# Optimization experiments

Hardware: AMD Instinct MI355X
Metric: run time of the kernel (lower is better)

## Reference

```python
import jax, jax.numpy as jnp
import numpy as np

B, S, DIM, HEADS, HD, FF = 2, 2048, 1024, 16, 64, 4096
PREV, MAX_SEQ, THETA, POS_BIAS_MAX, EPS = 1024, 4096, 10000.0, 2.0, 1e-6


def _freqs_cos_sin():
    inv = 1.0 / THETA ** (np.arange(0, HD, 2)[: HD // 2].astype(np.float32) / HD)
    f = np.outer(np.arange(MAX_SEQ, dtype=np.float32), inv)
    return jnp.asarray(np.cos(f), jnp.float32), jnp.asarray(np.sin(f), jnp.float32)


def setup_inputs():
    key = jax.random.key(0)
    ks = jax.random.split(key, 16)
    lin = lambda k, o, i: 0.02 * jax.random.normal(k, (o, i), jnp.float32)
    cos, sin = _freqs_cos_sin()
    return {
        "x": jax.random.normal(ks[0], (B, S, DIM), jnp.float32),
        "cache_k": jax.random.normal(ks[1], (B, HEADS, PREV, HD), jnp.float32),
        "cache_v": jax.random.normal(ks[2], (B, HEADS, PREV, HD), jnp.float32),
        "cos": cos, "sin": sin,
        "attn_norm_w": jnp.ones((DIM,), jnp.float32),
        "ffn_norm_w": jnp.ones((DIM,), jnp.float32),
        "wq": lin(ks[3], DIM, DIM), "bq": jnp.zeros((DIM,), jnp.float32),
        "wk": lin(ks[4], DIM, DIM), "bk": jnp.zeros((DIM,), jnp.float32),
        "wv": lin(ks[5], DIM, DIM), "bv": jnp.zeros((DIM,), jnp.float32),
        "wo": lin(ks[6], DIM, DIM), "bo": jnp.zeros((DIM,), jnp.float32),
        "w_gate": lin(ks[7], FF, DIM), "b_gate": jnp.zeros((FF,), jnp.float32),
        "w_value": lin(ks[8], FF, DIM), "b_value": jnp.zeros((FF,), jnp.float32),
        "w_proj": lin(ks[9], DIM, FF), "b_proj": jnp.zeros((DIM,), jnp.float32),
        "cache_limit": 3072,
    }


def _rmsnorm(h, w):
    return h * jax.lax.rsqrt(jnp.mean(h * h, axis=-1, keepdims=True) + EPS) * w


def _rope(t, cos, sin):
    # t: [B,H,L,HD]; cos/sin: [L, HD//2]; rotate interleaved pairs (complex mult)
    t2 = t.reshape(t.shape[:-1] + (HD // 2, 2))
    x0, x1 = t2[..., 0], t2[..., 1]
    c = cos[None, None]
    s = sin[None, None]
    out = jnp.stack([x0 * c - x1 * s, x0 * s + x1 * c], axis=-1)
    return out.reshape(t.shape)


def _forward(x, cache_k, cache_v, cos, sin, attn_norm_w, ffn_norm_w, wq, bq, wk, bk, wv, bv, wo, bo, w_gate, b_gate, w_value, b_value, w_proj, b_proj, cache_limit):
    b, s, d = x.shape
    h = _rmsnorm(x, attn_norm_w)
    shape4 = lambda t: t.reshape(b, s, HEADS, HD).transpose(0, 2, 1, 3)  # [B,H,S,HD]
    q = shape4(h @ wq.T + bq)
    k_new = shape4(h @ wk.T + bk)
    v_new = shape4(h @ wv.T + bv)
    k_all = jnp.concatenate([cache_k, k_new], axis=2)
    v_all = jnp.concatenate([cache_v, v_new], axis=2)
    if cache_limit > 0:
        k_all = k_all[:, :, -cache_limit:, :]
        v_all = v_all[:, :, -cache_limit:, :]
    total = k_all.shape[2]
    prev = total - s
    # RoPE: q at absolute positions prev..prev+s-1, keys at 0..total-1 (mod cache len)
    pos_q = (jnp.arange(s) + prev) % MAX_SEQ
    pos_k = jnp.arange(total) % MAX_SEQ
    q = _rope(q, cos[pos_q], sin[pos_q])
    k = _rope(k_all, cos[pos_k], sin[pos_k])
    # linear positional bias + causal mask over the new-token block only
    slope = POS_BIAS_MAX / max(total - 1, 1)
    j = jnp.arange(total, dtype=jnp.float32)[None, :]
    i_abs = (prev + jnp.arange(s, dtype=jnp.float32))[:, None]
    bias = slope * (j - i_abs)  # [s, total]
    causal = (jnp.arange(total)[None, :] - prev) > jnp.arange(s)[:, None]
    mask = jnp.where(causal, -jnp.inf, bias)
    scores = jnp.einsum('bhsd,bhtd->bhst', q, k) / jnp.sqrt(jnp.float32(HD)) + mask
    attn = jax.nn.softmax(scores, axis=-1)
    ctx = jnp.einsum('bhst,bhtd->bhsd', attn, v_all)
    ctx = ctx.transpose(0, 2, 1, 3).reshape(b, s, d)
    x = x + ctx @ wo.T + bo
    h2 = _rmsnorm(x, ffn_norm_w)
    gated = jax.nn.silu(h2 @ w_gate.T + b_gate) * (h2 @ w_value.T + b_value)
    return x + gated @ w_proj.T + b_proj


def reference(x, cache_k, cache_v, cos, sin, attn_norm_w, ffn_norm_w, wq, bq, wk, bk, wv, bv, wo, bo, w_gate, b_gate, w_value, b_value, w_proj, b_proj, cache_limit):
    return _forward(x, cache_k, cache_v, cos, sin, attn_norm_w, ffn_norm_w, wq, bq, wk, bk, wv, bv, wo, bo, w_gate, b_gate, w_value, b_value, w_proj, b_proj, cache_limit)
```

## Files before the change

### kernel.cpp

```cpp
#include <hip/hip_runtime.h>
#include <stdint.h>

typedef unsigned short u16;
typedef unsigned int   u32;
typedef __bf16 bf16x8 __attribute__((ext_vector_type(8)));
typedef float  f32x4  __attribute__((ext_vector_type(4)));
typedef u32    u32x4  __attribute__((ext_vector_type(4)));
typedef u32    u32x2  __attribute__((ext_vector_type(2)));

#define B_SZ  2
#define S_LEN 2048
#define NH    16
#define HD    64
#define DIM   1024
#define FF    4096
#define T_LEN 3072
#define PREV  1024
#define MROWS (B_SZ * S_LEN)
#define LOG2E 1.44269504f

#define MFMA16 __builtin_amdgcn_mfma_f32_16x16x32_bf16

__device__ __forceinline__ u16 f2bf(float f) {
  u32 u = __builtin_bit_cast(u32, f);
  u32 r = u + 0x7FFFu + ((u >> 16) & 1u);
  return (u16)(r >> 16);
}
__device__ __forceinline__ float bf2f(u16 h) {
  u32 u = ((u32)h) << 16;
  return __builtin_bit_cast(float, u);
}
__device__ __forceinline__ u32 cvtpk(float lo, float hi) {
  u32 r;
  asm("v_cvt_pk_bf16_f32 %0, %1, %2" : "=v"(r) : "v"(lo), "v"(hi));
  return r;
}

__device__ __forceinline__ void gl_lds16(const void* g, void* l) {
  __builtin_amdgcn_global_load_lds(
      (const __attribute__((address_space(1))) u32*)g,
      (__attribute__((address_space(3))) u32*)l, 16, 0, 0);
}

__global__ __launch_bounds__(256) void cvt_kernel(const float* __restrict__ src,
                                                  u16* __restrict__ dst, int n4) {
  int i = blockIdx.x * 256 + threadIdx.x;
  const int stride = gridDim.x * 256;
  for (; i < n4; i += stride) {
    f32x4 v = *(const f32x4*)&src[(long)i * 4];
    u32x2 o;
    o[0] = (u32)f2bf(v[0]) | ((u32)f2bf(v[1]) << 16);
    o[1] = (u32)f2bf(v[2]) | ((u32)f2bf(v[3]) << 16);
    *(u32x2*)&dst[(long)i * 4] = o;
  }
}

__global__ __launch_bounds__(256) void cvt_ilv_kernel(const float* __restrict__ wg,
                                                      const float* __restrict__ wval,
                                                      u16* __restrict__ dst) {
  int i = blockIdx.x * 256 + threadIdx.x;
  const int stride = gridDim.x * 256;
  const int upr = DIM / 4;
  for (; i < FF * upr; i += stride) {
    int j = i / upr;
    int c = (i - j * upr) * 4;
    f32x4 g = *(const f32x4*)&wg[(long)j * DIM + c];
    f32x4 v = *(const f32x4*)&wval[(long)j * DIM + c];
    u32x2 og, ov;
    og[0] = (u32)f2bf(g[0]) | ((u32)f2bf(g[1]) << 16);
    og[1] = (u32)f2bf(g[2]) | ((u32)f2bf(g[3]) << 16);
    ov[0] = (u32)f2bf(v[0]) | ((u32)f2bf(v[1]) << 16);
    ov[1] = (u32)f2bf(v[2]) | ((u32)f2bf(v[3]) << 16);
    *(u32x2*)&dst[((long)2 * j) * DIM + c] = og;
    *(u32x2*)&dst[((long)2 * j + 1) * DIM + c] = ov;
  }
}

__global__ __launch_bounds__(256) void bias_ilv_kernel(const float* __restrict__ bg,
                                                       const float* __restrict__ bval,
                                                       float* __restrict__ dst) {
  int i = blockIdx.x * 256 + threadIdx.x;
  if (i < FF) {
    dst[2 * i] = bg[i];
    dst[2 * i + 1] = bval[i];
  }
}

__global__ __launch_bounds__(256) void rmsnorm_kernel(const float* __restrict__ x,
                                                      const float* __restrict__ w,
                                                      u16* __restrict__ out) {
  const int row = blockIdx.x;
  const int tid = threadIdx.x;
  const long base = (long)row * DIM + tid * 4;
  f32x4 v = *(const f32x4*)&x[base];
  float ss = v[0] * v[0] + v[1] * v[1] + v[2] * v[2] + v[3] * v[3];
#pragma unroll
  for (int d = 1; d <= 32; d <<= 1) ss += __shfl_xor(ss, d, 64);
  __shared__ float red[4];
  if ((tid & 63) == 0) red[tid >> 6] = ss;
  __syncthreads();
  float tot = red[0] + red[1] + red[2] + red[3];
  const float sc = rsqrtf(tot * (1.f / (float)DIM) + 1e-6f);
  f32x4 wv4 = *(const f32x4*)&w[tid * 4];
  u32x2 o;
  o[0] = (u32)f2bf(v[0] * sc * wv4[0]) | ((u32)f2bf(v[1] * sc * wv4[1]) << 16);
  o[1] = (u32)f2bf(v[2] * sc * wv4[2]) | ((u32)f2bf(v[3] * sc * wv4[3]) << 16);
  *(u32x2*)&out[base] = o;
}

template <int EPI>
__global__ __launch_bounds__(256) void gemm_bt(const u16* __restrict__ A,
                                               const u16* __restrict__ Bw,
                                               const float* __restrict__ bias,
                                               const float* __restrict__ resid,
                                               u16* __restrict__ out_bf,
                                               float* __restrict__ out_f,
                                               int N, int K) {
  __shared__ __align__(16) u16 As[2][128 * 32];
  __shared__ __align__(16) u16 Bs[2][128 * 32];
  const int tid = threadIdx.x;
  const int lane = tid & 63;
  const int wv = tid >> 6;
  const int wr = wv >> 1, wc = wv & 1;
  const long m0 = (long)blockIdx.y * 128;
  const long n0 = (long)blockIdx.x * 128;

  const int arow = tid >> 2;
  const int acol = (tid & 3) << 3;
  const u16* ag = A + (m0 + arow) * K + acol;
  const u16* bg = Bw + (n0 + arow) * K + acol;
  const long hK = (long)64 * K;

  f32x4 acc[4][4] = {};
  const int l15 = lane & 15;
  const int lhi = lane >> 4;
  const int aoff0 = (wr * 64 + l15) * 32 + lhi * 8;
  const int boff0 = (wc * 64 + l15) * 32 + lhi * 8;
  const int nk = K >> 5;

  gl_lds16(ag, &As[0][tid * 8]);
  gl_lds16(ag + hK, &As[0][2048 + tid * 8]);
  gl_lds16(bg, &Bs[0][tid * 8]);
  gl_lds16(bg + hK, &Bs[0][2048 + tid * 8]);
  __syncthreads();

  for (int t = 0; t < nk; ++t) {
    const int cur = t & 1, nxt = cur ^ 1;
    if (t + 1 < nk) {
      const int k1 = (t + 1) << 5;
      gl_lds16(ag + k1, &As[nxt][tid * 8]);
      gl_lds16(ag + k1 + hK, &As[nxt][2048 + tid * 8]);
      gl_lds16(bg + k1, &Bs[nxt][tid * 8]);
      gl_lds16(bg + k1 + hK, &Bs[nxt][2048 + tid * 8]);
    }
    bf16x8 af[4], bfr[4];
#pragma unroll
    for (int i = 0; i < 4; ++i) af[i] = *(const bf16x8*)&As[cur][aoff0 + i * 16 * 32];
#pragma unroll
    for (int j = 0; j < 4; ++j) bfr[j] = *(const bf16x8*)&Bs[cur][boff0 + j * 16 * 32];
    __builtin_amdgcn_s_setprio(1);
#pragma unroll
    for (int i = 0; i < 4; ++i)
#pragma unroll
      for (int j = 0; j < 4; ++j)
        acc[i][j] = MFMA16(af[i], bfr[j], acc[i][j], 0, 0, 0);
    __builtin_amdgcn_s_setprio(0);
    __syncthreads();
  }

#pragma unroll
  for (int i = 0; i < 4; ++i) {
    const long row0 = m0 + wr * 64 + i * 16 + lhi * 4;
#pragma unroll
    for (int j = 0; j < 4; ++j) {
      const long col = n0 + wc * 64 + j * 16 + l15;
      const float bb = bias[col];
#pragma unroll
      for (int r = 0; r < 4; ++r) {
        float v = acc[i][j][r] + bb;
        if (EPI == 2) {
          float other = __shfl_xor(v, 1, 64);
          if (!(l15 & 1)) {
            float s = v / (1.f + __expf(-v)) * other;
            out_bf[(row0 + r) * (N >> 1) + (col >> 1)] = f2bf(s);
          }
        } else {
          const long idx = (row0 + r) * N + col;
          if (EPI == 0) out_bf[idx] = f2bf(v);
          else          out_f[idx] = resid[idx] + v;
        }
      }
    }
  }
}

__global__ __launch_bounds__(256) void rope_q_kernel(const u16* __restrict__ qkv,
                                                     const float* __restrict__ cosT,
                                                     const float* __restrict__ sinT,
                                                     u16* __restrict__ Q) {
  int idx = blockIdx.x * 256 + threadIdx.x;
  int u = idx & 7;
  int s = (idx >> 3) & (S_LEN - 1);
  int bh = idx >> 14;
  int b = bh >> 4, h = bh & 15;
  int pos = PREV + s;
  const float SC = 0.125f * LOG2E;
  const u16* src = qkv + ((long)(b * S_LEN + s)) * (3 * DIM) + h * HD + u * 8;
  u32x4 d = *(const u32x4*)src;
  f32x4 cv = *(const f32x4*)&cosT[(long)pos * 32 + u * 4];
  f32x4 sv = *(const f32x4*)&sinT[(long)pos * 32 + u * 4];
  u32x4 o;
#pragma unroll
  for (int p = 0; p < 4; ++p) {
    float x0 = bf2f((u16)(d[p] & 0xffff));
    float x1 = bf2f((u16)(d[p] >> 16));
    float y0 = (x0 * cv[p] - x1 * sv[p]) * SC;
    float y1 = (x0 * sv[p] + x1 * cv[p]) * SC;
    o[p] = (u32)f2bf(y0) | ((u32)f2bf(y1) << 16);
  }
  *(u32x4*)&Q[((long)bh * S_LEN + s) * HD + u * 8] = o;
}

__global__ __launch_bounds__(256) void rope_k_kernel(const u16* __restrict__ qkv,
                                                     const float* __restrict__ cache_k,
                                                     const float* __restrict__ cosT,
                                                     const float* __restrict__ sinT,
                                                     u16* __restrict__ Kall) {
  int idx = blockIdx.x * 256 + threadIdx.x;
  int u = idx & 7;
  int t2 = idx >> 3;
  int j = t2 % T_LEN;
  int bh = t2 / T_LEN;
  int b = bh >> 4, h = bh & 15;
  float e[8];
  if (j < PREV) {
    const float* src = cache_k + ((long)bh * PREV + j) * HD + u * 8;
    f32x4 a = *(const f32x4*)src;
    f32x4 c = *(const f32x4*)(src + 4);
    e[0] = a[0]; e[1] = a[1]; e[2] = a[2]; e[3] = a[3];
    e[4] = c[0]; e[5] = c[1]; e[6] = c[2]; e[7] = c[3];
  } else {
    const u16* src = qkv + ((long)(b * S_LEN + (j - PREV))) * (3 * DIM) + DIM + h * HD + u * 8;
    u32x4 d = *(const u32x4*)src;
#pragma unroll
    for (int p = 0; p < 4; ++p) {
      e[2 * p] = bf2f((u16)(d[p] & 0xffff));
      e[2 * p + 1] = bf2f((u16)(d[p] >> 16));
    }
  }
  f32x4 cv = *(const f32x4*)&cosT[(long)j * 32 + u * 4];
  f32x4 sv = *(const f32x4*)&sinT[(long)j * 32 + u * 4];
  u32x4 o;
#pragma unroll
  for (int p = 0; p < 4; ++p) {
    float y0 = e[2 * p] * cv[p] - e[2 * p + 1] * sv[p];
    float y1 = e[2 * p] * sv[p] + e[2 * p + 1] * cv[p];
    o[p] = (u32)f2bf(y0) | ((u32)f2bf(y1) << 16);
  }
  *(u32x4*)&Kall[((long)bh * T_LEN + j) * HD + (u ^ (j & 7)) * 8] = o;
}

__global__ __launch_bounds__(256) void build_vt_kernel(const u16* __restrict__ qkv,
                                                       const float* __restrict__ cache_v,
                                                       u16* __restrict__ Vtg) {
  int idx = blockIdx.x * 256 + threadIdx.x;
  int hd = idx & 63;
  int t2 = idx >> 6;
  int kb = t2 % 384;
  int bh = t2 / 384;
  int b = bh >> 4, h = bh & 15;
  int key0 = kb * 8;
  u16 vals[8];
  if (key0 < PREV) {
#pragma unroll
    for (int i = 0; i < 8; ++i)
      vals[i] = f2bf(cache_v[((long)bh * PREV + key0 + i) * HD + hd]);
  } else {
#pragma unroll
    for (int i = 0; i < 8; ++i)
      vals[i] = qkv[((long)(b * S_LEN + key0 + i - PREV)) * (3 * DIM) + 2 * DIM + h * HD + hd];
  }
  u32x4 o;
#pragma unroll
  for (int p = 0; p < 4; ++p)
    o[p] = (u32)vals[2 * p] | ((u32)vals[2 * p + 1] << 16);
  const int span = kb >> 3;
  const int u = (kb & 7) ^ (hd & 7);
  *(u32x4*)&Vtg[((long)bh * HD + hd) * T_LEN + span * 64 + u * 8] = o;
}

__global__ __launch_bounds__(256, 4) void attn_kernel(const u16* __restrict__ Q,
                                                      const u16* __restrict__ Kg,
                                                      const u16* __restrict__ Vtg,
                                                      u16* __restrict__ ctx, float slope2) {
  __shared__ __align__(16) u16 Ks[2][64 * 64];
  __shared__ __align__(16) u16 Vs[2][64 * 64];
  __shared__ __align__(16) u16 Ps[4][16 * 64];

  const int tid = threadIdx.x;
  const int lane = tid & 63;
  const int wv = tid >> 6;
  const int l15 = lane & 15;
  const int lhi = lane >> 4;
  const int c7 = l15 & 7;
  const int bh = blockIdx.x;
  const int qt = blockIdx.y;
  const int b = bh >> 4, h = bh & 15;
  const int q0 = qt * 64;
  const int nt = (PREV + q0 + 64) >> 6;

  const long qrow = (long)bh * S_LEN + q0 + wv * 16 + l15;
  bf16x8 aq0 = *(const bf16x8*)&Q[qrow * HD + lhi * 8];
  bf16x8 aq1 = *(const bf16x8*)&Q[qrow * HD + 32 + lhi * 8];

  const long kgb = (long)bh * T_LEN * HD;
  const long vgb = (long)bh * HD * T_LEN;
  const int srow = tid >> 3;
  const int sunit = (tid & 7) * 8;

  gl_lds16(&Kg[kgb + (long)srow * HD + sunit], &Ks[0][tid * 8]);
  gl_lds16(&Kg[kgb + (long)(srow + 32) * HD + sunit], &Ks[0][2048 + tid * 8]);
  gl_lds16(&Vtg[vgb + (long)srow * T_LEN + sunit], &Vs[0][tid * 8]);
  gl_lds16(&Vtg[vgb + (long)(srow + 32) * T_LEN + sunit], &Vs[0][2048 + tid * 8]);
  __syncthreads();

  f32x4 o[4] = {};
  float mrun = -1e30f, lrun = 0.f;
  const int iabs = PREV + q0 + wv * 16 + l15;
  u16* Pw = &Ps[wv][0];

  for (int t = 0; t < nt; ++t) {
    const int cur = t & 1, nxt = cur ^ 1;
    const int kt0 = t << 6;
    if (t + 1 < nt) {
      const int kn = kt0 + 64;
      gl_lds16(&Kg[kgb + (long)(kn + srow) * HD + sunit], &Ks[nxt][tid * 8]);
      gl_lds16(&Kg[kgb + (long)(kn + srow + 32) * HD + sunit], &Ks[nxt][2048 + tid * 8]);
      gl_lds16(&Vtg[vgb + (long)srow * T_LEN + kn + sunit], &Vs[nxt][tid * 8]);
      gl_lds16(&Vtg[vgb + (long)(srow + 32) * T_LEN + kn + sunit], &Vs[nxt][2048 + tid * 8]);
    }

    f32x4 sf[4];
    __builtin_amdgcn_s_setprio(1);
#pragma unroll
    for (int jf = 0; jf < 4; ++jf) {
      const int krow = jf * 16 + l15;
      bf16x8 ak0 = *(const bf16x8*)&Ks[cur][krow * 64 + ((lhi ^ c7) * 8)];
      bf16x8 ak1 = *(const bf16x8*)&Ks[cur][krow * 64 + (((4 + lhi) ^ c7) * 8)];
      f32x4 s = {};
      s = MFMA16(ak0, aq0, s, 0, 0, 0);
      s = MFMA16(ak1, aq1, s, 0, 0, 0);
      sf[jf] = s;
    }
    __builtin_amdgcn_s_setprio(0);

    const bool masked = (t == nt - 1);
#pragma unroll
    for (int jf = 0; jf < 4; ++jf)
#pragma unroll
      for (int r = 0; r < 4; ++r) {
        const int jcol = kt0 + jf * 16 + 4 * lhi + r;
        float s_ = sf[jf][r] + slope2 * (float)(jcol - iabs);
        sf[jf][r] = (masked && jcol > iabs) ? -1e30f : s_;
      }

    float t0 = fmaxf(fmaxf(sf[0][0], sf[0][1]), fmaxf(sf[0][2], sf[0][3]));
    float t1 = fmaxf(fmaxf(sf[1][0], sf[1][1]), fmaxf(sf[1][2], sf[1][3]));
    float t2 = fmaxf(fmaxf(sf[2][0], sf[2][1]), fmaxf(sf[2][2], sf[2][3]));
    float t3 = fmaxf(fmaxf(sf[3][0], sf[3][1]), fmaxf(sf[3][2], sf[3][3]));
    float pmax = fmaxf(fmaxf(t0, t1), fmaxf(t2, t3));
    pmax = fmaxf(pmax, __shfl_xor(pmax, 16, 64));
    pmax = fmaxf(pmax, __shfl_xor(pmax, 32, 64));

    if (!__all(pmax - mrun <= 8.f)) {
      float mnew = fmaxf(mrun, pmax);
      float scl = exp2f(mrun - mnew);
      mrun = mnew;
      lrun *= scl;
#pragma unroll
      for (int r = 0; r < 4; ++r) {
        float sr = __shfl(scl, 4 * lhi + r, 64);
#pragma unroll
        for (int hf = 0; hf < 4; ++hf) o[hf][r] *= sr;
      }
    }

    float ps = 0.f;
#pragma unroll
    for (int jf = 0; jf < 4; ++jf) {
      f32x4 p;
#pragma unroll
      for (int r = 0; r < 4; ++r) {
        p[r] = exp2f(sf[jf][r] - mrun);
        ps += p[r];
      }
      u32x2 pw2;
      pw2[0] = cvtpk(p[0], p[1]);
      pw2[1] = cvtpk(p[2], p[3]);
      const int u = (2 * jf + (lhi >> 1)) ^ c7;
      *(u32x2*)&Pw[l15 * 64 + u * 8 + (lhi & 1) * 4] = pw2;
    }
    ps += __shfl_xor(ps, 16, 64);
    ps += __shfl_xor(ps, 32, 64);
    lrun += ps;

    bf16x8 pa0 = *(const bf16x8*)&Pw[l15 * 64 + ((lhi ^ c7) * 8)];
    bf16x8 pa1 = *(const bf16x8*)&Pw[l15 * 64 + (((4 + lhi) ^ c7) * 8)];
    __builtin_amdgcn_s_setprio(1);
#pragma unroll
    for (int hf = 0; hf < 4; ++hf) {
      const int vrow = hf * 16 + l15;
      bf16x8 bv0 = *(const bf16x8*)&Vs[cur][vrow * 64 + ((lhi ^ c7) * 8)];
      bf16x8 bv1 = *(const bf16x8*)&Vs[cur][vrow * 64 + (((4 + lhi) ^ c7) * 8)];
      o[hf] = MFMA16(pa0, bv0, o[hf], 0, 0, 0);
      o[hf] = MFMA16(pa1, bv1, o[hf], 0, 0, 0);
    }
    __builtin_amdgcn_s_setprio(0);
    __syncthreads();
  }

#pragma unroll
  for (int r = 0; r < 4; ++r) {
    const float inv = 1.f / __shfl(lrun, 4 * lhi + r, 64);
    const long srow_ = (long)b * S_LEN + q0 + wv * 16 + 4 * lhi + r;
#pragma unroll
    for (int hf = 0; hf < 4; ++hf)
      ctx[srow_ * DIM + h * HD + hf * 16 + l15] = f2bf(o[hf][r] * inv);
  }
}

extern "C" void kernel_launch(void* const* d_in, const int* in_sizes, int n_in,
                              void* d_out, int out_size, void* d_ws, size_t ws_size,
                              hipStream_t stream) {
  (void)in_sizes; (void)n_in; (void)out_size; (void)ws_size;
  const float* x       = (const float*)d_in[0];
  const float* cache_k = (const float*)d_in[1];
  const float* cache_v = (const float*)d_in[2];
  const float* cosT    = (const float*)d_in[3];
  const float* sinT    = (const float*)d_in[4];
  const float* attn_w  = (const float*)d_in[5];
  const float* ffn_w   = (const float*)d_in[6];
  const float* wq      = (const float*)d_in[7];
  const float* bq      = (const float*)d_in[8];
  const float* wk      = (const float*)d_in[9];
  const float* bk      = (const float*)d_in[10];
  const float* wv_     = (const float*)d_in[11];
  const float* bv      = (const float*)d_in[12];
  const float* wo      = (const float*)d_in[13];
  const float* bo      = (const float*)d_in[14];
  const float* wg      = (const float*)d_in[15];
  const float* bg      = (const float*)d_in[16];
  const float* wval    = (const float*)d_in[17];
  const float* bval    = (const float*)d_in[18];
  const float* wp      = (const float*)d_in[19];
  const float* bp      = (const float*)d_in[20];
  float* out = (float*)d_out;

  char* w = (char*)d_ws;
  size_t off = 0;
  auto alloc = [&](size_t bytes) -> char* {
    char* p = w + off;
    off += (bytes + 255) & ~(size_t)255;
    return p;
  };
  u16*   wqkv_bf  = (u16*)alloc((size_t)3 * DIM * DIM * 2);
  u16*   wo_bf    = (u16*)alloc((size_t)DIM * DIM * 2);
  u16*   wgv_bf   = (u16*)alloc((size_t)2 * FF * DIM * 2);
  u16*   wproj_bf = (u16*)alloc((size_t)DIM * FF * 2);
  float* bqkv     = (float*)alloc((size_t)3 * DIM * 4);
  float* bgv      = (float*)alloc((size_t)2 * FF * 4);
  float* x2       = (float*)alloc((size_t)MROWS * DIM * 4);
  char* AR = alloc((size_t)117440512);
  u16* qkv   = (u16*)(AR + 0);
  u16* Qb    = (u16*)(AR + 25165824);
  u16* Kb    = (u16*)(AR + 33554432);
  u16* Vtg   = (u16*)(AR + 46137344);
  u16* h1    = (u16*)(AR + 58720256);
  u16* ctx   = (u16*)(AR + 0);
  u16* h2    = (u16*)(AR + 8388608);
  u16* gated = (u16*)(AR + 16777216);

  cvt_kernel<<<512, 256, 0, stream>>>(wq, wqkv_bf, DIM * DIM / 4);
  cvt_kernel<<<512, 256, 0, stream>>>(wk, wqkv_bf + DIM * DIM, DIM * DIM / 4);
  cvt_kernel<<<512, 256, 0, stream>>>(wv_, wqkv_bf + 2 * DIM * DIM, DIM * DIM / 4);
  cvt_kernel<<<512, 256, 0, stream>>>(wo, wo_bf, DIM * DIM / 4);
  cvt_ilv_kernel<<<1024, 256, 0, stream>>>(wg, wval, wgv_bf);
  cvt_kernel<<<1024, 256, 0, stream>>>(wp, wproj_bf, DIM * FF / 4);
  bias_ilv_kernel<<<16, 256, 0, stream>>>(bg, bval, bgv);
  hipMemcpyAsync(bqkv, bq, DIM * 4, hipMemcpyDeviceToDevice, stream);
  hipMemcpyAsync(bqkv + DIM, bk, DIM * 4, hipMemcpyDeviceToDevice, stream);
  hipMemcpyAsync(bqkv + 2 * DIM, bv, DIM * 4, hipMemcpyDeviceToDevice, stream);

  rmsnorm_kernel<<<MROWS, 256, 0, stream>>>(x, attn_w, h1);
  gemm_bt<0><<<dim3(24, 32), 256, 0, stream>>>(h1, wqkv_bf, bqkv, nullptr, qkv, nullptr,
                                               3 * DIM, DIM);
  rope_q_kernel<<<2048, 256, 0, stream>>>(qkv, cosT, sinT, Qb);
  rope_k_kernel<<<3072, 256, 0, stream>>>(qkv, cache_k, cosT, sinT, Kb);
  build_vt_kernel<<<3072, 256, 0, stream>>>(qkv, cache_v, Vtg);
  attn_kernel<<<dim3(B_SZ * NH, S_LEN / 64), 256, 0, stream>>>(
      Qb, Kb, Vtg, ctx, (2.0f / (float)(T_LEN - 1)) * LOG2E);
  gemm_bt<1><<<dim3(8, 32), 256, 0, stream>>>(ctx, wo_bf, bo, x, nullptr, x2, DIM, DIM);
  rmsnorm_kernel<<<MROWS, 256, 0, stream>>>(x2, ffn_w, h2);
  gemm_bt<2><<<dim3(64, 32), 256, 0, stream>>>(h2, wgv_bf, bgv, nullptr, gated, nullptr,
                                               2 * FF, DIM);
  gemm_bt<1><<<dim3(8, 32), 256, 0, stream>>>(gated, wproj_bf, bp, x2, nullptr, out,
                                              DIM, FF);
}
```

Before: 405.2 us.

## Triple-buffer GEMM LDS pipeline and use narrower N tiles for DIM-output GEMMs

The GEMM kernel moves from double to triple buffering of the LDS tiles, with loads issued two K-steps ahead and explicit vmcnt waits plus barriers in place of a full __syncthreads. An NB template parameter allows 64-wide N tiles, which the two N=1024 GEMMs (output projection and FFN down projection) now use to double their grid from 256 to 512 blocks and fill more CUs. The cost is more LDS per block, which may reduce occupancy, and less data reuse per block on the narrow tiles.

```diff
diff --git a/kernel.cpp b/kernel.cpp
--- a/kernel.cpp
+++ b/kernel.cpp
@@ -108,7 +108,7 @@
   *(u32x2*)&out[base] = o;
 }
 
-template <int EPI>
+template <int EPI, int NB>
 __global__ __launch_bounds__(256) void gemm_bt(const u16* __restrict__ A,
                                                const u16* __restrict__ Bw,
                                                const float* __restrict__ bias,
@@ -116,14 +116,17 @@
                                                u16* __restrict__ out_bf,
                                                float* __restrict__ out_f,
                                                int N, int K) {
-  __shared__ __align__(16) u16 As[2][128 * 32];
-  __shared__ __align__(16) u16 Bs[2][128 * 32];
+  constexpr int BHALF = NB / 64;
+  constexpr int NFR = NB / 32;
+  constexpr int LPT = 2 + BHALF;
+  __shared__ __align__(16) u16 As[3][128 * 32];
+  __shared__ __align__(16) u16 Bs[3][NB * 32];
   const int tid = threadIdx.x;
   const int lane = tid & 63;
   const int wv = tid >> 6;
   const int wr = wv >> 1, wc = wv & 1;
   const long m0 = (long)blockIdx.y * 128;
-  const long n0 = (long)blockIdx.x * 128;
+  const long n0 = (long)blockIdx.x * NB;
 
   const int arow = tid >> 2;
   const int acol = (tid & 3) << 3;
@@ -131,49 +134,62 @@
   const u16* bg = Bw + (n0 + arow) * K + acol;
   const long hK = (long)64 * K;
 
-  f32x4 acc[4][4] = {};
+  f32x4 acc[4][NFR] = {};
   const int l15 = lane & 15;
   const int lhi = lane >> 4;
   const int aoff0 = (wr * 64 + l15) * 32 + lhi * 8;
-  const int boff0 = (wc * 64 + l15) * 32 + lhi * 8;
+  const int boff0 = (wc * (NB / 2) + l15) * 32 + lhi * 8;
   const int nk = K >> 5;
 
-  gl_lds16(ag, &As[0][tid * 8]);
-  gl_lds16(ag + hK, &As[0][2048 + tid * 8]);
-  gl_lds16(bg, &Bs[0][tid * 8]);
-  gl_lds16(bg + hK, &Bs[0][2048 + tid * 8]);
-  __syncthreads();
+  auto stage = [&](int t, int buf) {
+    const int k0 = t << 5;
+    gl_lds16(ag + k0, &As[buf][tid * 8]);
+    gl_lds16(ag + k0 + hK, &As[buf][2048 + tid * 8]);
+    gl_lds16(bg + k0, &Bs[buf][tid * 8]);
+    if (BHALF == 2) gl_lds16(bg + k0 + hK, &Bs[buf][2048 + tid * 8]);
+  };
+
+  stage(0, 0);
+  stage(1, 1);
+  asm volatile("s_waitcnt vmcnt(%0)" ::"n"(LPT) : "memory");
+  __builtin_amdgcn_s_barrier();
+  asm volatile("" ::: "memory");
+  __builtin_amdgcn_sched_barrier(0);
 
   for (int t = 0; t < nk; ++t) {
-    const int cur = t & 1, nxt = cur ^ 1;
-    if (t + 1 < nk) {
-      const int k1 = (t + 1) << 5;
-      gl_lds16(ag + k1, &As[nxt][tid * 8]);
-      gl_lds16(ag + k1 + hK, &As[nxt][2048 + tid * 8]);
-      gl_lds16(bg + k1, &Bs[nxt][tid * 8]);
-      gl_lds16(bg + k1 + hK, &Bs[nxt][2048 + tid * 8]);
-    }
-    bf16x8 af[4], bfr[4];
-#pragma unroll
-    for (int i = 0; i < 4; ++i) af[i] = *(const bf16x8*)&As[cur][aoff0 + i * 16 * 32];
-#pragma unroll
-    for (int j = 0; j < 4; ++j) bfr[j] = *(const bf16x8*)&Bs[cur][boff0 + j * 16 * 32];
+    const int cb = t % 3;
+    if (t + 2 < nk) stage(t + 2, (t + 2) % 3);
+    bf16x8 af[4], bfr[NFR];
+#pragma unroll
+    for (int i = 0; i < 4; ++i) af[i] = *(const bf16x8*)&As[cb][aoff0 + i * 16 * 32];
+#pragma unroll
+    for (int j = 0; j < NFR; ++j) bfr[j] = *(const bf16x8*)&Bs[cb][boff0 + j * 16 * 32];
     __builtin_amdgcn_s_setprio(1);
 #pragma unroll
     for (int i = 0; i < 4; ++i)
 #pragma unroll
-      for (int j = 0; j < 4; ++j)
+      for (int j = 0; j < NFR; ++j)
         acc[i][j] = MFMA16(af[i], bfr[j], acc[i][j], 0, 0, 0);
     __builtin_amdgcn_s_setprio(0);
-    __syncthreads();
+    if (t + 2 < nk) {
+      asm volatile("s_waitcnt vmcnt(%0)" ::"n"(LPT) : "memory");
+      __builtin_amdgcn_s_barrier();
+      asm volatile("" ::: "memory");
+      __builtin_amdgcn_sched_barrier(0);
+    } else if (t + 1 < nk) {
+      asm volatile("s_waitcnt vmcnt(0)" ::: "memory");
+      __builtin_amdgcn_s_barrier();
+      asm volatile("" ::: "memory");
+      __builtin_amdgcn_sched_barrier(0);
+    }
   }
 
 #pragma unroll
   for (int i = 0; i < 4; ++i) {
     const long row0 = m0 + wr * 64 + i * 16 + lhi * 4;
 #pragma unroll
-    for (int j = 0; j < 4; ++j) {
-      const long col = n0 + wc * 64 + j * 16 + l15;
+    for (int j = 0; j < NFR; ++j) {
+      const long col = n0 + wc * (NB / 2) + j * 16 + l15;
       const float bb = bias[col];
 #pragma unroll
       for (int r = 0; r < 4; ++r) {
@@ -492,17 +508,18 @@
   hipMemcpyAsync(bqkv + 2 * DIM, bv, DIM * 4, hipMemcpyDeviceToDevice, stream);
 
   rmsnorm_kernel<<<MROWS, 256, 0, stream>>>(x, attn_w, h1);
-  gemm_bt<0><<<dim3(24, 32), 256, 0, stream>>>(h1, wqkv_bf, bqkv, nullptr, qkv, nullptr,
-                                               3 * DIM, DIM);
+  gemm_bt<0, 128><<<dim3(24, 32), 256, 0, stream>>>(h1, wqkv_bf, bqkv, nullptr, qkv,
+                                                    nullptr, 3 * DIM, DIM);
   rope_q_kernel<<<2048, 256, 0, stream>>>(qkv, cosT, sinT, Qb);
   rope_k_kernel<<<3072, 256, 0, stream>>>(qkv, cache_k, cosT, sinT, Kb);
   build_vt_kernel<<<3072, 256, 0, stream>>>(qkv, cache_v, Vtg);
   attn_kernel<<<dim3(B_SZ * NH, S_LEN / 64), 256, 0, stream>>>(
       Qb, Kb, Vtg, ctx, (2.0f / (float)(T_LEN - 1)) * LOG2E);
-  gemm_bt<1><<<dim3(8, 32), 256, 0, stream>>>(ctx, wo_bf, bo, x, nullptr, x2, DIM, DIM);
+  gemm_bt<1, 64><<<dim3(16, 32), 256, 0, stream>>>(ctx, wo_bf, bo, x, nullptr, x2,
+                                                   DIM, DIM);
   rmsnorm_kernel<<<MROWS, 256, 0, stream>>>(x2, ffn_w, h2);
-  gemm_bt<2><<<dim3(64, 32), 256, 0, stream>>>(h2, wgv_bf, bgv, nullptr, gated, nullptr,
-                                               2 * FF, DIM);
-  gemm_bt<1><<<dim3(8, 32), 256, 0, stream>>>(gated, wproj_bf, bp, x2, nullptr, out,
-                                              DIM, FF);
-}
+  gemm_bt<2, 128><<<dim3(64, 32), 256, 0, stream>>>(h2, wgv_bf, bgv, nullptr, gated,
+                                                    nullptr, 2 * FF, DIM);
+  gemm_bt<1, 64><<<dim3(16, 32), 256, 0, stream>>>(gated, wproj_bf, bp, x2, nullptr, out,
+                                                   DIM, FF);
+}
```

After: 397.7 us. Within noise of the previous version (-1.9%).
